# Performance work log

Hardware: AMD Instinct MI355X
Metric: run time of the kernel (lower is better)

The kernel has to match this reference:

```python
import jax, jax.numpy as jnp
import numpy as np

B = 65536      # batch
C = 1000       # num_classes
D = 256        # feat_dim


def _l2norm(x, eps=1e-12):
    # matches F.normalize(dim=1): v / max(||v||_2, eps)
    n = jnp.linalg.norm(x, axis=1, keepdims=True)
    return x / jnp.maximum(n, eps)


def setup_inputs() -> dict:
    key = jax.random.key(0)
    k1, k2, k3, k4, k5 = jax.random.split(key, 5)
    bound = 1.0 / np.sqrt(D)
    X = jax.random.normal(k1, (B, D), dtype=jnp.float32)
    labels = jax.random.randint(k2, (B,), 0, C)
    signatures = jax.random.uniform(k3, (C, D), dtype=jnp.float32, minval=-bound, maxval=bound)
    b_means = jax.random.uniform(k4, (1, D), dtype=jnp.float32, minval=-bound, maxval=bound)
    b_covs = jax.random.normal(k5, (D, D), dtype=jnp.float32)
    return {"X": X, "labels": labels, "signatures": signatures,
            "b_means": b_means, "b_covs": b_covs}


def reference(X, labels, signatures, b_means, b_covs):
    # SVD-based whitening of background covariance (tiny DxD)
    cov = b_covs @ b_covs.T
    U, eig, _ = jnp.linalg.svd(cov)
    DU = (eig ** -0.5)[:, None] * U.T              # diag(eig^-1/2) @ U^T, [D, D]
    xHat = _l2norm((X - b_means) @ DU.T)           # [B, D]
    sHat = _l2norm(signatures @ DU.T)              # [C, D]
    ACE_targets = xHat @ sHat.T                    # [B, C] cosine scores
    labels = labels.astype(jnp.int32)
    numerator = jnp.take_along_axis(ACE_targets, labels[:, None], axis=1)[:, 0]
    # denominator = exp(true) + sum(exp(others)) == sum over all classes
    loss = -jnp.mean(numerator - jax.nn.logsumexp(ACE_targets, axis=1))
    return (loss, ACE_targets)
```

## Files before the change

### kernel.cpp

```cpp
#include <hip/hip_runtime.h>
#include <hip/hip_bf16.h>
#include <math.h>

#define D_ 256
#define B_ 65536
#define C_ 1000

typedef _Float16 f16x8 __attribute__((ext_vector_type(8)));
typedef float f32x4 __attribute__((ext_vector_type(4)));

__global__ __launch_bounds__(256) void cov_kernel(const float* __restrict__ bc,
                                                  double* __restrict__ C64,
                                                  double* __restrict__ acc,
                                                  unsigned int* __restrict__ counter) {
  __shared__ float Ash[32][260];
  __shared__ float Bsh2[32][260];
  const int b = blockIdx.x, bi = b >> 3, bj = b & 7;
  const int e = threadIdx.x;
  if (b == 0 && e == 0) { *acc = 0.0; *counter = 0u; }
#pragma unroll
  for (int s = 0; s < 32; ++s) {
    int lin = s * 256 + e;
    int rr = lin >> 8, cc = lin & 255;
    Ash[rr][cc] = bc[(bi * 32 + rr) * 256 + cc];
    Bsh2[rr][cc] = bc[(bj * 32 + rr) * 256 + cc];
  }
  __syncthreads();
  const int tx = e & 15, ty = e >> 4;
  double a00 = 0, a01 = 0, a10 = 0, a11 = 0;
#pragma unroll 8
  for (int k = 0; k < 256; ++k) {
    double ar0 = (double)Ash[ty][k], ar1 = (double)Ash[ty + 16][k];
    double br0 = (double)Bsh2[tx][k], br1 = (double)Bsh2[tx + 16][k];
    a00 += ar0 * br0; a01 += ar0 * br1;
    a10 += ar1 * br0; a11 += ar1 * br1;
  }
  const int r0 = bi * 32, c0 = bj * 32;
  C64[(size_t)(r0 + ty) * D_ + c0 + tx] = a00;
  C64[(size_t)(r0 + ty) * D_ + c0 + tx + 16] = a01;
  C64[(size_t)(r0 + ty + 16) * D_ + c0 + tx] = a10;
  C64[(size_t)(r0 + ty + 16) * D_ + c0 + tx + 16] = a11;
}

__global__ __launch_bounds__(256, 1) void chol_panel(double* __restrict__ A, int p) {
  const int j0 = p * 64;
  const int r = threadIdx.x;
  __shared__ double raw[2][64];
  double pr[64];
  const bool act = (r >= j0);
  const bool inpanel = act && (r < j0 + 64);
  if (act) {
#pragma unroll
    for (int k = 0; k < 64; ++k) pr[k] = A[(size_t)r * D_ + j0 + k];
  }
  if (inpanel) raw[0][r - j0] = pr[0];
  __syncthreads();
#pragma unroll
  for (int j = 0; j < 64; ++j) {
    const int col = j0 + j;
    const double d2 = raw[j & 1][j];
    double rs = (double)rsqrtf((float)d2);
    rs = rs * (1.5 - 0.5 * d2 * rs * rs);
    rs = rs * (1.5 - 0.5 * d2 * rs * rs);
    if (r >= col) {
      const double lr_ = pr[j] * rs;
      pr[j] = lr_;
#pragma unroll
      for (int k = j + 1; k < 64; ++k) pr[k] -= lr_ * (raw[j & 1][k] * rs);
    }
    if (j < 63) {
      if (r > col && r < j0 + 64) raw[(j + 1) & 1][r - j0] = pr[j + 1];
    }
    __syncthreads();
  }
  if (act) {
    const int kmax = (r - j0 < 63) ? (r - j0) : 63;
#pragma unroll
    for (int k = 0; k < 64; ++k)
      if (k <= kmax) A[(size_t)r * D_ + j0 + k] = pr[k];
  }
}

__global__ __launch_bounds__(256) void chol_trail(double* __restrict__ A, int p) {
  const int j0 = p * 64;
  const int t0 = j0 + 64;
  int b = blockIdx.x, I = 0;
  while (b >= I + 1) { b -= I + 1; ++I; }
  const int J = b;
  const int r0 = t0 + I * 64, c0 = t0 + J * 64;
  __shared__ double LR[64][67];
  __shared__ double LC[64][67];
  const int tid = threadIdx.x;
  for (int e = tid; e < 64 * 64; e += 256) {
    int rr = e >> 6, cc = e & 63;
    LR[rr][cc] = A[(size_t)(r0 + rr) * D_ + j0 + cc];
    LC[rr][cc] = A[(size_t)(c0 + rr) * D_ + j0 + cc];
  }
  __syncthreads();
  const int tx = tid & 15, ty = tid >> 4;
  double acc[4][4];
#pragma unroll
  for (int i = 0; i < 4; ++i)
#pragma unroll
    for (int j = 0; j < 4; ++j) acc[i][j] = 0.0;
#pragma unroll 4
  for (int k = 0; k < 64; ++k) {
    double a_[4], b_[4];
#pragma unroll
    for (int i = 0; i < 4; ++i) a_[i] = LR[ty + 16 * i][k];
#pragma unroll
    for (int j = 0; j < 4; ++j) b_[j] = LC[tx + 16 * j][k];
#pragma unroll
    for (int i = 0; i < 4; ++i)
#pragma unroll
      for (int j = 0; j < 4; ++j) acc[i][j] += a_[i] * b_[j];
  }
#pragma unroll
  for (int i = 0; i < 4; ++i) {
    const int grow = r0 + ty + 16 * i;
#pragma unroll
    for (int j = 0; j < 4; ++j) {
      const int gcol = c0 + tx + 16 * j;
      A[(size_t)grow * D_ + gcol] -= acc[i][j];
    }
  }
}

__global__ __launch_bounds__(256) void inv_kernel(const double* __restrict__ L,
                                                  _Float16* __restrict__ WbP,
                                                  _Float16* __restrict__ WbT) {
  const int c = blockIdx.x;
  const int tid = threadIdx.x;
  __shared__ double w[D_];
  __shared__ double rdi[D_];
  __shared__ double rhs[32];
  __shared__ double Ldd[32][33];
  w[tid] = 0.0;
  rdi[tid] = 1.0 / L[(size_t)tid * D_ + tid];
  __syncthreads();
  const int q0 = c >> 5;
  for (int q = q0; q < 8; ++q) {
    const int i0 = q * 32;
    const int ii = tid >> 3, s = tid & 7;
    const int i = i0 + ii;
    double part = 0.0;
    for (int k = c + s; k < i0; k += 8) part += L[(size_t)i * D_ + k] * w[k];
    part += __shfl_xor(part, 1, 64);
    part += __shfl_xor(part, 2, 64);
    part += __shfl_xor(part, 4, 64);
    if (s == 0) rhs[ii] = ((i == c) ? 1.0 : 0.0) - part;
    for (int e = tid; e < 32 * 32; e += 256) {
      int rr = e >> 5, cc = e & 31;
      Ldd[rr][cc] = L[(size_t)(i0 + rr) * D_ + i0 + cc];
    }
    __syncthreads();
    if (tid < 32) {
      double x = rhs[tid];
      double v = 0.0;
      for (int j = 0; j < 32; ++j) {
        double xj = __shfl(x, j, 64);
        double wj = xj * rdi[i0 + j];
        if (tid == j) v = wj;
        if (tid > j) x -= Ldd[tid][j] * wj;
      }
      w[i0 + tid] = v;
    }
    __syncthreads();
  }
  _Float16 h = (_Float16)(float)w[tid];
  WbT[(size_t)c * D_ + tid] = h;
  {
    const int g = tid >> 4, lrr = tid & 15;
    const int ks = c >> 5, lqq = (c >> 3) & 3, jj = c & 7;
    WbP[(size_t)(g * 8 + ks) * 512 + (size_t)(lqq * 16 + lrr) * 8 + jj] = h;
  }
}

__global__ void sig_kernel(const float* __restrict__ S, const _Float16* __restrict__ WbT,
                           _Float16* __restrict__ sHatP) {
  int c = blockIdx.x, i = threadIdx.x;
  const int g = c >> 4, lr = c & 15;
  const int ks = i >> 5, lq = (i >> 3) & 3, jj = i & 7;
  const size_t off = (size_t)(g * 8 + ks) * 512 + (size_t)(lq * 16 + lr) * 8 + jj;
  if (c >= C_) { sHatP[off] = (_Float16)0.0f; return; }
  __shared__ float srow[D_];
  __shared__ float wred[4];
  srow[i] = S[c * D_ + i];
  __syncthreads();
  float t = 0.f;
  for (int k = 0; k < D_; ++k) t += (float)WbT[k * D_ + i] * srow[k];
  float ss = t * t;
#pragma unroll
  for (int d = 1; d < 64; d <<= 1) ss += __shfl_xor(ss, d, 64);
  if ((i & 63) == 0) wred[i >> 6] = ss;
  __syncthreads();
  float tot = wred[0] + wred[1] + wred[2] + wred[3];
  float rn = 1.0f / fmaxf(sqrtf(tot), 1e-12f);
  sHatP[off] = (_Float16)(t * rn);
}

__global__ __launch_bounds__(1024) void ace_kernel(const float* __restrict__ X,
                                                   const float* __restrict__ means,
                                                   const _Float16* __restrict__ WbP,
                                                   const _Float16* __restrict__ sHatP,
                                                   const int* __restrict__ labels,
                                                   float* __restrict__ out,
                                                   double* __restrict__ acc_loss,
                                                   unsigned int* __restrict__ counter) {
  __shared__ __align__(16) char ldsraw[132096];
  __shared__ float msh[D_];
  __shared__ float part[64];
  _Float16* const Wsh = (_Float16*)ldsraw;
  char* const xsC = ldsraw;
  _Float16* const Bsh = (_Float16*)ldsraw;
  float* const xferAll = (float*)(ldsraw + 65536);
  float* const outACE = out + 1;

  const int tid = threadIdx.x;
  const int wid = tid >> 6, l = tid & 63, lr = l & 15, lq = l >> 4;
  const int rowbase = blockIdx.x * 256;
  const int wrow = rowbase + wid * 16;
  const int arow = wrow + lr;

  if (tid < 256) msh[tid] = means[tid];
#pragma unroll
  for (int s = 0; s < 8; ++s) {
    const int off = (wid * 8 + s) * 512;
    __builtin_amdgcn_global_load_lds(
        (const __attribute__((address_space(1))) unsigned int*)(WbP + off + l * 8),
        (__attribute__((address_space(3))) unsigned int*)(Wsh + off), 16, 0, 0);
  }
  __syncthreads();

  f16x8 af[8];
#pragma unroll
  for (int ks = 0; ks < 8; ++ks) {
    const float* xp = X + (size_t)arow * D_ + lq * 8 + ks * 32;
    const float4 x0 = *(const float4*)(xp);
    const float4 x1 = *(const float4*)(xp + 4);
    const int mb = lq * 8 + ks * 32;
    af[ks][0] = (_Float16)(x0.x - msh[mb + 0]);
    af[ks][1] = (_Float16)(x0.y - msh[mb + 1]);
    af[ks][2] = (_Float16)(x0.z - msh[mb + 2]);
    af[ks][3] = (_Float16)(x0.w - msh[mb + 3]);
    af[ks][4] = (_Float16)(x1.x - msh[mb + 4]);
    af[ks][5] = (_Float16)(x1.y - msh[mb + 5]);
    af[ks][6] = (_Float16)(x1.z - msh[mb + 6]);
    af[ks][7] = (_Float16)(x1.w - msh[mb + 7]);
  }
  f32x4 wacc[16];
#pragma unroll
  for (int u = 0; u < 16; ++u) wacc[u] = (f32x4){0.f, 0.f, 0.f, 0.f};
  {
    const _Float16* wb = Wsh + (size_t)l * 8;
#pragma unroll
    for (int ks = 0; ks < 8; ++ks) {
#pragma unroll
      for (int u = 0; u < 16; ++u) {
        f16x8 bf = *(const f16x8*)(wb + (u * 8 + ks) * 512);
        wacc[u] = __builtin_amdgcn_mfma_f32_16x16x32_f16(af[ks], bf, wacc[u], 0, 0, 0);
      }
    }
  }
  float ss[4] = {0.f, 0.f, 0.f, 0.f};
#pragma unroll
  for (int u = 0; u < 16; ++u)
#pragma unroll
    for (int j = 0; j < 4; ++j) ss[j] += wacc[u][j] * wacc[u][j];
#pragma unroll
  for (int d = 1; d < 16; d <<= 1) {
#pragma unroll
    for (int j = 0; j < 4; ++j) ss[j] += __shfl_xor(ss[j], d, 64);
  }
  float rx[4];
#pragma unroll
  for (int j = 0; j < 4; ++j) rx[j] = 1.0f / fmaxf(sqrtf(ss[j]), 1e-12f);

  __syncthreads();

#pragma unroll
  for (int u = 0; u < 16; ++u) {
#pragma unroll
    for (int j = 0; j < 4; ++j) {
      const int rowl = wid * 16 + lq * 4 + j;
      const int byte = (rowl * 512 + (u * 16 + lr) * 2) ^ ((rowl & 7) << 4);
      *(_Float16*)(xsC + byte) = (_Float16)wacc[u][j];
    }
  }
  __syncthreads();
  f16x8 a[8];
  {
    const int rowA = wid * 16 + lr;
#pragma unroll
    for (int ks = 0; ks < 8; ++ks) {
      const int byte = (rowA * 512 + ks * 64 + lq * 16) ^ ((rowA & 7) << 4);
      a[ks] = *(const f16x8*)(xsC + byte);
    }
  }
  __syncthreads();

  int lab[4]; float ssum[4], num[4];
#pragma unroll
  for (int j = 0; j < 4; ++j) {
    lab[j] = labels[wrow + lq * 4 + j];
    ssum[j] = 0.f; num[j] = 0.f;
  }

#define STAGE(bufi, hci) do {                                                        \
    const _Float16* _src = sHatP + (size_t)(hci) * 16384;                            \
    _Float16* _dst = Bsh + (size_t)(bufi) * 16384;                                   \
    _Pragma("unroll")                                                                \
    for (int _s = 0; _s < 2; ++_s) {                                                 \
      const int _off = wid * 1024 + _s * 512;                                        \
      __builtin_amdgcn_global_load_lds(                                              \
          (const __attribute__((address_space(1))) unsigned int*)(_src + _off + l * 8), \
          (__attribute__((address_space(3))) unsigned int*)(_dst + _off), 16, 0, 0); \
    } } while (0)

  float* const xf = xferAll + wid * 1040;

  STAGE(0, 0);
  __syncthreads();
  int buf = 0;
  for (int hc = 0; hc < 16; ++hc) {
    if (hc < 15) {
      STAGE(buf ^ 1, hc + 1);
      __builtin_amdgcn_sched_barrier(0);
    }
    const _Float16* bb = Bsh + (size_t)buf * 16384 + (size_t)l * 8;
    f32x4 acc[4];
#pragma unroll
    for (int t = 0; t < 4; ++t) acc[t] = (f32x4){0.f, 0.f, 0.f, 0.f};
#pragma unroll
    for (int ks = 0; ks < 8; ++ks) {
#pragma unroll
      for (int t = 0; t < 4; ++t) {
        f16x8 bf = *(const f16x8*)(bb + (t * 8 + ks) * 512);
        acc[t] = __builtin_amdgcn_mfma_f32_16x16x32_f16(a[ks], bf, acc[t], 0, 0, 0);
      }
    }
#pragma unroll
    for (int t = 0; t < 4; ++t) {
      const int col = hc * 64 + t * 16 + lr;
#pragma unroll
      for (int j = 0; j < 4; ++j) {
        float v = acc[t][j] * rx[j];
        ssum[j] += __expf(v - 1.0f);
        num[j] = (col == lab[j]) ? v : num[j];
        xf[(lq * 4 + j) * 65 + t * 16 + lr] = v;
      }
    }
    {
      const int colS = hc * 64 + l;
      if (colS < C_) {
#pragma unroll
        for (int r = 0; r < 16; ++r)
          outACE[(size_t)(wrow + r) * C_ + colS] = xf[r * 65 + l];
      }
    }
    if (hc < 15) {
      __builtin_amdgcn_sched_barrier(0);
      asm volatile("s_waitcnt vmcnt(16)" ::: "memory");
      __builtin_amdgcn_s_barrier();
      __builtin_amdgcn_sched_barrier(0);
    }
    buf ^= 1;
  }
#undef STAGE

#pragma unroll
  for (int d2 = 1; d2 < 16; d2 <<= 1) {
#pragma unroll
    for (int j = 0; j < 4; ++j) {
      ssum[j] += __shfl_xor(ssum[j], d2, 64);
      num[j]  += __shfl_xor(num[j], d2, 64);
    }
  }
  if (lr == 0) {
    const float padcorr = 24.0f * __expf(-1.0f);
    float contrib = 0.f;
#pragma unroll
    for (int j = 0; j < 4; ++j)
      contrib += num[j] - (1.0f + __logf(ssum[j] - padcorr));
    part[wid * 4 + lq] = contrib;
  }
  __syncthreads();
  if (tid == 0) {
    float s = 0.f;
#pragma unroll
    for (int p2 = 0; p2 < 64; ++p2) s += part[p2];
    atomicAdd(acc_loss, (double)s);
    __threadfence();
    unsigned int old = atomicAdd(counter, 1u);
    if (old == (unsigned int)(gridDim.x - 1)) {
      __threadfence();
      double tot = atomicAdd(acc_loss, 0.0);
      out[0] = (float)(-tot / (double)B_);
    }
  }
}

extern "C" void kernel_launch(void* const* d_in, const int* in_sizes, int n_in,
                              void* d_out, int out_size, void* d_ws, size_t ws_size,
                              hipStream_t stream) {
  const float* X      = (const float*)d_in[0];
  const int*   labels = (const int*)d_in[1];
  const float* S      = (const float*)d_in[2];
  const float* means  = (const float*)d_in[3];
  const float* bc     = (const float*)d_in[4];
  float* out = (float*)d_out;

  char* w = (char*)d_ws;
  double*       acc   = (double*)(w + 0);
  unsigned int* cnt   = (unsigned int*)(w + 128);
  double*       C64   = (double*)(w + 256);
  _Float16*     WbP   = (_Float16*)(w + 524544);
  _Float16*     WbT   = (_Float16*)(w + 655616);
  _Float16*     sHatP = (_Float16*)(w + 786688);

  cov_kernel<<<64, 256, 0, stream>>>(bc, C64, acc, cnt);
  for (int p = 0; p < 4; ++p) {
    chol_panel<<<1, 256, 0, stream>>>(C64, p);
    int nt = 3 - p;
    if (nt > 0) chol_trail<<<nt * (nt + 1) / 2, 256, 0, stream>>>(C64, p);
  }
  inv_kernel<<<256, 256, 0, stream>>>(C64, WbP, WbT);
  sig_kernel<<<1024, 256, 0, stream>>>(S, WbT, sHatP);
  ace_kernel<<<256, 1024, 0, stream>>>(X, means, WbP, sHatP, labels, out, acc, cnt);
}
```

Measured before the change: 358.6 us.

## Halve ace_kernel block size, split whitening staging, write scores directly

The ACE kernel now uses 512-thread blocks covering 128 rows, in a grid of 512 blocks. It cuts LDS to 64 KB so several blocks can share a CU. The whitening matrix is staged into LDS in two halves, which adds extra barriers. The LDS transpose buffer for the score output is removed, and each lane now writes its MFMA results straight to global memory with strided, less coalesced stores. The goal is higher occupancy and less LDS traffic, at the cost of store coalescing and extra synchronisation.

```diff
diff --git a/kernel.cpp b/kernel.cpp
--- a/kernel.cpp
+++ b/kernel.cpp
@@ -199,37 +199,41 @@
   sHatP[off] = (_Float16)(t * rn);
 }
 
-__global__ __launch_bounds__(1024) void ace_kernel(const float* __restrict__ X,
-                                                   const float* __restrict__ means,
-                                                   const _Float16* __restrict__ WbP,
-                                                   const _Float16* __restrict__ sHatP,
-                                                   const int* __restrict__ labels,
-                                                   float* __restrict__ out,
-                                                   double* __restrict__ acc_loss,
-                                                   unsigned int* __restrict__ counter) {
-  __shared__ __align__(16) char ldsraw[132096];
+__global__ __launch_bounds__(512, 4) void ace_kernel(const float* __restrict__ X,
+                                                     const float* __restrict__ means,
+                                                     const _Float16* __restrict__ WbP,
+                                                     const _Float16* __restrict__ sHatP,
+                                                     const int* __restrict__ labels,
+                                                     float* __restrict__ out,
+                                                     double* __restrict__ acc_loss,
+                                                     unsigned int* __restrict__ counter) {
+  __shared__ __align__(16) char ldsraw[65536];
   __shared__ float msh[D_];
-  __shared__ float part[64];
+  __shared__ float part[32];
   _Float16* const Wsh = (_Float16*)ldsraw;
   char* const xsC = ldsraw;
   _Float16* const Bsh = (_Float16*)ldsraw;
-  float* const xferAll = (float*)(ldsraw + 65536);
   float* const outACE = out + 1;
 
   const int tid = threadIdx.x;
   const int wid = tid >> 6, l = tid & 63, lr = l & 15, lq = l >> 4;
-  const int rowbase = blockIdx.x * 256;
+  const int rowbase = blockIdx.x * 128;
   const int wrow = rowbase + wid * 16;
   const int arow = wrow + lr;
 
   if (tid < 256) msh[tid] = means[tid];
-#pragma unroll
-  for (int s = 0; s < 8; ++s) {
-    const int off = (wid * 8 + s) * 512;
-    __builtin_amdgcn_global_load_lds(
-        (const __attribute__((address_space(1))) unsigned int*)(WbP + off + l * 8),
-        (__attribute__((address_space(3))) unsigned int*)(Wsh + off), 16, 0, 0);
-  }
+
+#define STAGE_W(halfi) do {                                                          \
+    _Pragma("unroll")                                                                \
+    for (int _s = 0; _s < 8; ++_s) {                                                 \
+      const int _off = (wid * 8 + _s) * 512;                                         \
+      __builtin_amdgcn_global_load_lds(                                              \
+          (const __attribute__((address_space(1))) unsigned int*)                    \
+              (WbP + (size_t)(halfi) * 32768 + _off + l * 8),                        \
+          (__attribute__((address_space(3))) unsigned int*)(Wsh + _off), 16, 0, 0);  \
+    } } while (0)
+
+  STAGE_W(0);
   __syncthreads();
 
   f16x8 af[8];
@@ -248,6 +252,7 @@
     af[ks][6] = (_Float16)(x1.z - msh[mb + 6]);
     af[ks][7] = (_Float16)(x1.w - msh[mb + 7]);
   }
+
   f32x4 wacc[16];
 #pragma unroll
   for (int u = 0; u < 16; ++u) wacc[u] = (f32x4){0.f, 0.f, 0.f, 0.f};
@@ -256,12 +261,28 @@
 #pragma unroll
     for (int ks = 0; ks < 8; ++ks) {
 #pragma unroll
-      for (int u = 0; u < 16; ++u) {
+      for (int u = 0; u < 8; ++u) {
         f16x8 bf = *(const f16x8*)(wb + (u * 8 + ks) * 512);
         wacc[u] = __builtin_amdgcn_mfma_f32_16x16x32_f16(af[ks], bf, wacc[u], 0, 0, 0);
       }
     }
   }
+  __syncthreads();
+  STAGE_W(1);
+  __syncthreads();
+  {
+    const _Float16* wb = Wsh + (size_t)l * 8;
+#pragma unroll
+    for (int ks = 0; ks < 8; ++ks) {
+#pragma unroll
+      for (int u = 8; u < 16; ++u) {
+        f16x8 bf = *(const f16x8*)(wb + ((u - 8) * 8 + ks) * 512);
+        wacc[u] = __builtin_amdgcn_mfma_f32_16x16x32_f16(af[ks], bf, wacc[u], 0, 0, 0);
+      }
+    }
+  }
+#undef STAGE_W
+
   float ss[4] = {0.f, 0.f, 0.f, 0.f};
 #pragma unroll
   for (int u = 0; u < 16; ++u)
@@ -310,14 +331,14 @@
     const _Float16* _src = sHatP + (size_t)(hci) * 16384;                            \
     _Float16* _dst = Bsh + (size_t)(bufi) * 16384;                                   \
     _Pragma("unroll")                                                                \
-    for (int _s = 0; _s < 2; ++_s) {                                                 \
-      const int _off = wid * 1024 + _s * 512;                                        \
+    for (int _s = 0; _s < 4; ++_s) {                                                 \
+      const int _off = wid * 2048 + _s * 512;                                        \
       __builtin_amdgcn_global_load_lds(                                              \
           (const __attribute__((address_space(1))) unsigned int*)(_src + _off + l * 8), \
           (__attribute__((address_space(3))) unsigned int*)(_dst + _off), 16, 0, 0); \
     } } while (0)
 
-  float* const xf = xferAll + wid * 1040;
+  float* const outrow = outACE + (size_t)(wrow + lq * 4) * C_;
 
   STAGE(0, 0);
   __syncthreads();
@@ -342,20 +363,13 @@
 #pragma unroll
     for (int t = 0; t < 4; ++t) {
       const int col = hc * 64 + t * 16 + lr;
+      const bool valid = (col < C_);
 #pragma unroll
       for (int j = 0; j < 4; ++j) {
         float v = acc[t][j] * rx[j];
+        if (valid) outrow[(size_t)j * C_ + col] = v;
         ssum[j] += __expf(v - 1.0f);
         num[j] = (col == lab[j]) ? v : num[j];
-        xf[(lq * 4 + j) * 65 + t * 16 + lr] = v;
-      }
-    }
-    {
-      const int colS = hc * 64 + l;
-      if (colS < C_) {
-#pragma unroll
-        for (int r = 0; r < 16; ++r)
-          outACE[(size_t)(wrow + r) * C_ + colS] = xf[r * 65 + l];
       }
     }
     if (hc < 15) {
@@ -388,7 +402,7 @@
   if (tid == 0) {
     float s = 0.f;
 #pragma unroll
-    for (int p2 = 0; p2 < 64; ++p2) s += part[p2];
+    for (int p2 = 0; p2 < 32; ++p2) s += part[p2];
     atomicAdd(acc_loss, (double)s);
     __threadfence();
     unsigned int old = atomicAdd(counter, 1u);
@@ -426,5 +440,5 @@
   }
   inv_kernel<<<256, 256, 0, stream>>>(C64, WbP, WbT);
   sig_kernel<<<1024, 256, 0, stream>>>(S, WbT, sHatP);
-  ace_kernel<<<256, 1024, 0, stream>>>(X, means, WbP, sHatP, labels, out, acc, cnt);
-}
+  ace_kernel<<<512, 512, 0, stream>>>(X, means, WbP, sHatP, labels, out, acc, cnt);
+}
```

Result: slower. 368.0 us (+2.6%).

## Restructure Cholesky panel into blocked wavefront-shuffle factorization with TRSM

Applied to the files above, without the earlier changes.

Rewrites the Cholesky panel kernel so the 64x64 diagonal block is factored in two 32-column halves by the first wavefront using cross-lane shuffles instead of a block-wide barrier per column. The rows below the diagonal block are solved afterwards by triangular substitution against the factor stored in shared memory. This replaces 64 block barriers with a few, removing per-column synchronisation latency from a serial stage. The cost is more register pressure and a changed operation order in fp64, which may alter rounding slightly.

```diff
diff --git a/kernel.cpp b/kernel.cpp
--- a/kernel.cpp
+++ b/kernel.cpp
@@ -44,40 +44,100 @@
 
 __global__ __launch_bounds__(256, 1) void chol_panel(double* __restrict__ A, int p) {
   const int j0 = p * 64;
-  const int r = threadIdx.x;
-  __shared__ double raw[2][64];
-  double pr[64];
-  const bool act = (r >= j0);
-  const bool inpanel = act && (r < j0 + 64);
-  if (act) {
-#pragma unroll
-    for (int k = 0; k < 64; ++k) pr[k] = A[(size_t)r * D_ + j0 + k];
-  }
-  if (inpanel) raw[0][r - j0] = pr[0];
-  __syncthreads();
-#pragma unroll
-  for (int j = 0; j < 64; ++j) {
-    const int col = j0 + j;
-    const double d2 = raw[j & 1][j];
-    double rs = (double)rsqrtf((float)d2);
-    rs = rs * (1.5 - 0.5 * d2 * rs * rs);
-    rs = rs * (1.5 - 0.5 * d2 * rs * rs);
-    if (r >= col) {
-      const double lr_ = pr[j] * rs;
-      pr[j] = lr_;
-#pragma unroll
-      for (int k = j + 1; k < 64; ++k) pr[k] -= lr_ * (raw[j & 1][k] * rs);
-    }
-    if (j < 63) {
-      if (r > col && r < j0 + 64) raw[(j + 1) & 1][r - j0] = pr[j + 1];
-    }
-    __syncthreads();
-  }
-  if (act) {
-    const int kmax = (r - j0 < 63) ? (r - j0) : 63;
-#pragma unroll
-    for (int k = 0; k < 64; ++k)
-      if (k <= kmax) A[(size_t)r * D_ + j0 + k] = pr[k];
+  const int tid = threadIdx.x;
+  __shared__ double Lp[64][33];
+  __shared__ double rsv[32];
+  const int row = j0 + tid;
+  const bool active = (row < D_);
+  const bool diag = active && (tid < 64);
+
+  double x[32], y[32];
+  if (active) {
+#pragma unroll
+    for (int k = 0; k < 32; ++k) x[k] = A[(size_t)row * D_ + j0 + k];
+#pragma unroll
+    for (int k = 0; k < 32; ++k) y[k] = A[(size_t)row * D_ + j0 + 32 + k];
+  }
+
+  if (diag) {
+#pragma unroll
+    for (int j = 0; j < 32; ++j) {
+      const double d2 = __shfl(x[j], j, 64);
+      double rs = (double)rsqrtf((float)d2);
+      rs = rs * (1.5 - 0.5 * d2 * rs * rs);
+      rs = rs * (1.5 - 0.5 * d2 * rs * rs);
+      const double lr = x[j] * rs;
+      x[j] = lr;
+      if (tid == j) rsv[j] = rs;
+#pragma unroll
+      for (int k = j + 1; k < 32; ++k) {
+        const double lkj = __shfl(lr, k, 64);
+        x[k] -= lr * lkj;
+      }
+    }
+#pragma unroll
+    for (int k = 0; k < 32; ++k) Lp[tid][k] = x[k];
+  }
+  __syncthreads();
+
+  if (active && tid >= 64) {
+#pragma unroll
+    for (int j = 0; j < 32; ++j) {
+      const double wj = x[j] * rsv[j];
+      x[j] = wj;
+#pragma unroll
+      for (int k = j + 1; k < 32; ++k) x[k] -= wj * Lp[k][j];
+    }
+  }
+  if (active) {
+#pragma unroll
+    for (int c = 0; c < 32; ++c) {
+      double s = 0.0;
+#pragma unroll
+      for (int j = 0; j < 32; ++j) s += x[j] * Lp[32 + c][j];
+      y[c] -= s;
+    }
+  }
+  __syncthreads();
+
+  if (diag) {
+#pragma unroll
+    for (int j = 0; j < 32; ++j) {
+      const double d2 = __shfl(y[j], 32 + j, 64);
+      double rs = (double)rsqrtf((float)d2);
+      rs = rs * (1.5 - 0.5 * d2 * rs * rs);
+      rs = rs * (1.5 - 0.5 * d2 * rs * rs);
+      const double lr = y[j] * rs;
+      y[j] = lr;
+      if (tid == 32 + j) rsv[j] = rs;
+#pragma unroll
+      for (int k = j + 1; k < 32; ++k) {
+        const double lkj = __shfl(lr, 32 + k, 64);
+        y[k] -= lr * lkj;
+      }
+    }
+    if (tid >= 32) {
+#pragma unroll
+      for (int k = 0; k < 32; ++k) Lp[tid][k] = y[k];
+    }
+  }
+  __syncthreads();
+
+  if (active && tid >= 64) {
+#pragma unroll
+    for (int j = 0; j < 32; ++j) {
+      const double wj = y[j] * rsv[j];
+      y[j] = wj;
+#pragma unroll
+      for (int k = j + 1; k < 32; ++k) y[k] -= wj * Lp[32 + k][j];
+    }
+  }
+
+  if (active) {
+#pragma unroll
+    for (int k = 0; k < 32; ++k) A[(size_t)row * D_ + j0 + k] = x[k];
+#pragma unroll
+    for (int k = 0; k < 32; ++k) A[(size_t)row * D_ + j0 + 32 + k] = y[k];
   }
 }
 
```

Result: slower. 417.7 us (+16.5%).
